# Kernel optimization log

Measured on AMD Instinct MI355X. Metric: run time of the kernel, lower is better.

Reference implementation:

```python
import jax, jax.numpy as jnp
import numpy as np

POOL = 7        # adaptive max pool output size
STRIDE = 16.0   # feature stride of VGG16 conv5


def _bin_masks(lo, hi, size, nbins=POOL):
    """Boolean masks [R, nbins, size]: pixel p belongs to adaptive-pool bin i
    of the region [lo, hi). PyTorch AdaptiveMaxPool2d bin boundaries:
    start = floor(i*L/n), end = ceil((i+1)*L/n), L = hi - lo."""
    L = hi - lo                                   # [R]
    i = jnp.arange(nbins, dtype=jnp.int32)
    starts = lo[:, None] + (i[None, :] * L[:, None]) // nbins          # [R, nbins]
    ends = lo[:, None] + ((i[None, :] + 1) * L[:, None] + nbins - 1) // nbins
    pos = jnp.arange(size, dtype=jnp.int32)
    return (pos[None, None, :] >= starts[..., None]) & (pos[None, None, :] < ends[..., None])


def roi_pool(x, rois):
    """x: [1,C,H,W]; rois: [R,4] = (y1,x1,y2,x2) in image pixels.
    Returns [R, C, POOL, POOL], matching the per-ROI slice + AdaptiveMaxPool2d loop."""
    xf = x[0]                                     # [C,H,W]
    C, H, W = xf.shape
    h0 = (rois[:, 0] / STRIDE).astype(jnp.int32)
    h1 = (rois[:, 2] / STRIDE).astype(jnp.int32) + 1
    w0 = (rois[:, 1] / STRIDE).astype(jnp.int32)
    w1 = (rois[:, 3] / STRIDE).astype(jnp.int32) + 1
    mH = _bin_masks(h0, h1, H)                    # [R,7,H]
    mW = _bin_masks(w0, w1, W)                    # [R,7,W]
    NEG = jnp.finfo(xf.dtype).min
    # reduce over W per w-bin (small fixed loop over 7 bins keeps memory bounded)
    colmax = jnp.stack(
        [jnp.where(mW[:, wb][:, None, None, :], xf[None], NEG).max(-1) for wb in range(POOL)],
        axis=-1)                                  # [R,C,H,7]
    # reduce over H per h-bin
    pooled = jnp.stack(
        [jnp.where(mH[:, hb][:, None, :, None], colmax, NEG).max(2) for hb in range(POOL)],
        axis=2)                                   # [R,C,7,7]
    return pooled


def setup_inputs() -> dict:
    key = jax.random.key(0)
    ks = jax.random.split(key, 10)
    H_img, W_img = 16 * 37, 16 * 50
    x = jax.random.normal(ks[0], (1, 512, 37, 50), dtype=jnp.float32)
    R = 128
    y1 = jax.random.uniform(ks[1], (R,), minval=0.0, maxval=H_img - 32.0)
    x1 = jax.random.uniform(ks[2], (R,), minval=0.0, maxval=W_img - 32.0)
    hh = jax.random.uniform(ks[3], (R,), minval=16.0, maxval=256.0)
    ww = jax.random.uniform(ks[4], (R,), minval=16.0, maxval=256.0)
    y2 = jnp.minimum(y1 + hh, H_img - 1.0)
    x2 = jnp.minimum(x1 + ww, W_img - 1.0)
    rois = jnp.stack([y1, x1, y2, x2], axis=1).astype(jnp.float32)
    D_in, D_h = 512 * POOL * POOL, 4096
    n_class = 21
    W1 = jax.random.normal(ks[5], (D_in, D_h), dtype=jnp.float32) * 0.01
    b1 = jnp.zeros((D_h,), jnp.float32)
    W2 = jax.random.normal(ks[6], (D_h, D_h), dtype=jnp.float32) * 0.01
    b2 = jnp.zeros((D_h,), jnp.float32)
    Wloc = jax.random.normal(ks[7], (D_h, n_class * 4), dtype=jnp.float32) * 0.001
    bloc = jnp.zeros((n_class * 4,), jnp.float32)
    Wscore = jax.random.normal(ks[8], (D_h, n_class), dtype=jnp.float32) * 0.01
    bscore = jnp.zeros((n_class,), jnp.float32)
    return {"x": x, "rois": rois, "W1": W1, "b1": b1, "W2": W2, "b2": b2,
            "Wloc": Wloc, "bloc": bloc, "Wscore": Wscore, "bscore": bscore}


def reference(x, rois, W1, b1, W2, b2, Wloc, bloc, Wscore, bscore):
    pooled = roi_pool(x, rois)                    # [R,512,7,7]
    flat = pooled.reshape(pooled.shape[0], -1)    # [R,25088]
    fc6 = jax.nn.relu(flat @ W1 + b1)
    fc7 = jax.nn.relu(fc6 @ W2 + b2)
    roi_locs = fc7 @ Wloc + bloc                  # [R, n_class*4]
    roi_scores = fc7 @ Wscore + bscore            # [R, n_class]
    return roi_locs, roi_scores
```

## Files before the change

### kernel.cpp

```cpp
#include <hip/hip_runtime.h>
#include <hip/hip_bf16.h>


typedef __attribute__((ext_vector_type(8))) short bf16x8;
typedef __attribute__((ext_vector_type(4))) float f32x4;
typedef __attribute__((ext_vector_type(4))) short s16x4;

typedef const __attribute__((address_space(1))) void gvoid;
typedef __attribute__((address_space(3))) void lvoid;
#define GLD_LDS16(gp, lp) __builtin_amdgcn_global_load_lds((gvoid*)(gp), (lvoid*)(lp), 16, 0, 0)

#define WAITV8() { asm volatile("s_waitcnt vmcnt(8)" ::: "memory"); __builtin_amdgcn_sched_barrier(0); }
#define WAITV0() { asm volatile("s_waitcnt vmcnt(0)" ::: "memory"); __builtin_amdgcn_sched_barrier(0); }
#define BAR() { __builtin_amdgcn_sched_barrier(0); __builtin_amdgcn_s_barrier(); __builtin_amdgcn_sched_barrier(0); }

static __device__ __forceinline__ short f2bf(float f) {
  unsigned u = __builtin_bit_cast(unsigned, f);
  u += 0x7fffu + ((u >> 16) & 1u);
  return (short)(u >> 16);
}

__global__ __launch_bounds__(256) void roipool_kernel(
    const float* __restrict__ x, const float* __restrict__ rois,
    __hip_bfloat16* __restrict__ A) {
  const int cg = blockIdx.x;
  const int r  = blockIdx.y;
  const float y1 = rois[r*4+0], x1 = rois[r*4+1], y2 = rois[r*4+2], x2 = rois[r*4+3];
  const int h0 = (int)(y1 * 0.0625f);
  const int h1 = (int)(y2 * 0.0625f) + 1;
  const int w0 = (int)(x1 * 0.0625f);
  const int w1 = (int)(x2 * 0.0625f) + 1;
  const int Hh = h1 - h0, Ww = w1 - w0;
  const int n = Hh * Ww;
  __shared__ float tile[16][292];
  const int cl = threadIdx.x >> 4, i = threadIdx.x & 15;
  const int c = cg*16 + cl;
  const float* xc = x + c*1850 + h0*50 + w0;
  for (int p = i; p < n; p += 16) {
    int rr = p / Ww, cc = p - rr*Ww;
    tile[cl][p] = xc[rr*50 + cc];
  }
  __syncthreads();
  __hip_bfloat16* Arow = A + (size_t)r*25088 + c*49;
  for (int b = i; b < 49; b += 16) {
    int hb = b / 7, wb = b - hb*7;
    int rs = (hb*Hh)/7,  re = ((hb+1)*Hh + 6)/7;
    int cs = (wb*Ww)/7,  ce = ((wb+1)*Ww + 6)/7;
    float m = -3.402823466e38f;
    for (int rr2 = rs; rr2 < re; ++rr2)
      for (int cc2 = cs; cc2 < ce; ++cc2)
        m = fmaxf(m, tile[cl][rr2*Ww + cc2]);
    Arow[b] = __float2bfloat16(m);
  }
}

__global__ __launch_bounds__(256) void gemm_kernel(
    const __hip_bfloat16* __restrict__ A,
    const float* __restrict__ B,
    float* __restrict__ part,
    int K, int KC) {
  __shared__ short lA[2][8192];
  __shared__ float lB[2][4096];
  const int t = threadIdx.x;
  const int w = t >> 6, l = t & 63;
  const int bid = blockIdx.x;
  const int s  = bid & 7;
  const int nb = bid >> 3;
  const int kc0 = s * KC;
  const int Arow_bytes = K * 2;

  int aoff[4], boff[4];
#pragma unroll
  for (int p = 0; p < 4; ++p) {
    int o = (p*256 + t) * 16;
    int oa = o ^ (((o >> 7) & 7) << 4);
    aoff[p] = (oa >> 7) * Arow_bytes + (oa & 127);
    int ob = o ^ (((o >> 11) & 1) << 6);
    boff[p] = (ob >> 8) * 16384 + (ob & 255);
  }
  const int r15 = l & 15, kh = l >> 4;
  const int xa = (r15 & 7) << 4;
  const int aoj0 = r15*128 + ((kh*16) ^ xa);
  const int aoj1 = r15*128 + (((64) + kh*16) ^ xa);
  const int bo0  = ((kh*8)*256 + (w*16 + r15)*4) ^ ((kh & 1) << 6);

  const char* Ak = (const char*)A + kc0*2;
  const char* Bk = (const char*)B + (size_t)kc0*16384 + nb*256;

  f32x4 acc[8] = {};
  const int steps = KC >> 6;
  int cur = 0;

#pragma unroll
  for (int p = 0; p < 4; ++p) {
    GLD_LDS16(Ak + aoff[p], (char*)lA[0] + (p*256 + w*64)*16);
    GLD_LDS16(Bk + boff[p], (char*)lB[0] + (p*256 + w*64)*16);
  }
  Ak += 128; Bk += 64 * 16384;

  for (int st = 0; st < steps; ++st) {
    if (st + 1 < steps) {
      char* dA = (char*)lA[cur ^ 1];
      char* dB = (char*)lB[cur ^ 1];
#pragma unroll
      for (int p = 0; p < 4; ++p) {
        GLD_LDS16(Ak + aoff[p], dA + (p*256 + w*64)*16);
        GLD_LDS16(Bk + boff[p], dB + (p*256 + w*64)*16);
      }
      Ak += 128; Bk += 64 * 16384;
      WAITV8();
    } else {
      WAITV0();
    }
    BAR();
    const char* lAb = (const char*)lA[cur];
    const char* lBb = (const char*)lB[cur];
#pragma unroll
    for (int j = 0; j < 2; ++j) {
      const int ao = j ? aoj1 : aoj0;
      const int bo = (j ? 8192 : 0) + bo0;
      float bf[8];
#pragma unroll
      for (int i2 = 0; i2 < 8; ++i2)
        bf[i2] = *(const float*)(lBb + bo + i2*256);
      bf16x8 bfrag;
#pragma unroll
      for (int i2 = 0; i2 < 8; ++i2) bfrag[i2] = f2bf(bf[i2]);
#pragma unroll
      for (int mf = 0; mf < 8; ++mf) {
        bf16x8 afrag = *(const bf16x8*)(lAb + mf*2048 + ao);
        acc[mf] = __builtin_amdgcn_mfma_f32_16x16x32_bf16(afrag, bfrag, acc[mf], 0, 0, 0);
      }
    }
    BAR();
    cur ^= 1;
  }
  const int n = nb*64 + w*16 + r15;
  float* prow = part + (size_t)s*524288 + n;
#pragma unroll
  for (int mf = 0; mf < 8; ++mf) {
    int m0 = mf*16 + kh*4;
#pragma unroll
    for (int q = 0; q < 4; ++q)
      prow[(m0 + q)*4096] = acc[mf][q];
  }
}

__global__ __launch_bounds__(256) void reduce_kernel(
    const float* __restrict__ part, const float* __restrict__ bias,
    short* __restrict__ outp) {
  const int idx = (blockIdx.x*256 + threadIdx.x) * 4;
  f32x4 sum = {};
#pragma unroll
  for (int s2 = 0; s2 < 8; ++s2)
    sum += *(const f32x4*)(part + (size_t)s2*524288 + idx);
  sum += *(const f32x4*)(bias + (idx & 4095));
  s16x4 o;
#pragma unroll
  for (int q = 0; q < 4; ++q) o[q] = f2bf(fmaxf(sum[q], 0.f));
  *(s16x4*)(outp + idx) = o;
}

__global__ __launch_bounds__(512) void final_kernel(
    const float* __restrict__ part, const float* __restrict__ b2,
    const float* __restrict__ Wloc, const float* __restrict__ bloc,
    const float* __restrict__ Wscore, const float* __restrict__ bscore,
    float* __restrict__ out) {
  __shared__ float row[4096];
  __shared__ float psum[4][128];
  const int r = blockIdx.x, t = threadIdx.x;
  for (int ci = t; ci < 1024; ci += 512) {
    f32x4 sum = {};
#pragma unroll
    for (int s2 = 0; s2 < 8; ++s2)
      sum += *(const f32x4*)(part + (size_t)s2*524288 + r*4096 + ci*4);
    sum += *(const f32x4*)(b2 + ci*4);
    f32x4 o;
#pragma unroll
    for (int q = 0; q < 4; ++q) o[q] = fmaxf(sum[q], 0.f);
    *(f32x4*)&row[ci*4] = o;
  }
  __syncthreads();
  const int c = t & 127, ks = t >> 7;
  float acc = 0.f;
  if (c < 105) {
    const float* W; int stride, cc;
    if (c < 84) { W = Wloc; stride = 84; cc = c; }
    else        { W = Wscore; stride = 21; cc = c - 84; }
    const int k0 = ks * 1024;
#pragma unroll 4
    for (int k = k0; k < k0 + 1024; ++k)
      acc = fmaf(row[k], W[(size_t)k*stride + cc], acc);
  }
  psum[ks][c] = acc;
  __syncthreads();
  if (ks == 0 && c < 105) {
    float v = psum[0][c] + psum[1][c] + psum[2][c] + psum[3][c];
    if (c < 84) out[(size_t)r*84 + c] = v + bloc[c];
    else        out[10752 + (size_t)r*21 + (c - 84)] = v + bscore[c - 84];
  }
}

extern "C" void kernel_launch(void* const* d_in, const int* in_sizes, int n_in,
                              void* d_out, int out_size, void* d_ws, size_t ws_size,
                              hipStream_t stream) {
  const float* x      = (const float*)d_in[0];
  const float* rois   = (const float*)d_in[1];
  const float* W1     = (const float*)d_in[2];
  const float* b1     = (const float*)d_in[3];
  const float* W2     = (const float*)d_in[4];
  const float* b2     = (const float*)d_in[5];
  const float* Wloc   = (const float*)d_in[6];
  const float* bloc   = (const float*)d_in[7];
  const float* Wscore = (const float*)d_in[8];
  const float* bscore = (const float*)d_in[9];
  float* out = (float*)d_out;

  char* ws = (char*)d_ws;
  __hip_bfloat16* Apool = (__hip_bfloat16*)(ws);
  short*          fc6   = (short*)(ws + 6422528);
  float*          part  = (float*)(ws + 9568256);

  roipool_kernel<<<dim3(32, 128), 256, 0, stream>>>(x, rois, Apool);
  gemm_kernel<<<512, 256, 0, stream>>>(Apool, W1, part, 25088, 3136);
  reduce_kernel<<<512, 256, 0, stream>>>(part, b1, fc6);
  gemm_kernel<<<512, 256, 0, stream>>>((const __hip_bfloat16*)fc6, W2, part, 4096, 512);
  final_kernel<<<128, 512, 0, stream>>>(part, b2, Wloc, bloc, Wscore, bscore, out);
}
```

Measured before the change: 253.5 us.

## Use wider-N, shorter-K tiles and 16-way split-K for the fc6 GEMM

Adds a dedicated fc6 GEMM kernel whose tiles are 128 columns wide with a 32-deep K step, and which splits K 16 ways instead of 8. Each A fragment now feeds two MFMAs, so A is read from LDS and global memory half as often per output. The A swizzle and B layout are adjusted to match. In exchange there are twice as many partial-sum planes to write and reduce, and the reduce kernel now sums 16 planes.

```diff
diff --git a/kernel.cpp b/kernel.cpp
--- a/kernel.cpp
+++ b/kernel.cpp
@@ -11,6 +11,7 @@
 #define GLD_LDS16(gp, lp) __builtin_amdgcn_global_load_lds((gvoid*)(gp), (lvoid*)(lp), 16, 0, 0)
 
 #define WAITV8() { asm volatile("s_waitcnt vmcnt(8)" ::: "memory"); __builtin_amdgcn_sched_barrier(0); }
+#define WAITV6() { asm volatile("s_waitcnt vmcnt(6)" ::: "memory"); __builtin_amdgcn_sched_barrier(0); }
 #define WAITV0() { asm volatile("s_waitcnt vmcnt(0)" ::: "memory"); __builtin_amdgcn_sched_barrier(0); }
 #define BAR() { __builtin_amdgcn_sched_barrier(0); __builtin_amdgcn_s_barrier(); __builtin_amdgcn_sched_barrier(0); }
 
@@ -54,6 +55,101 @@
   }
 }
 
+__global__ __launch_bounds__(256) void gemm1_kernel(
+    const __hip_bfloat16* __restrict__ A,
+    const float* __restrict__ B,
+    float* __restrict__ part) {
+  __shared__ short lA[2][4096];
+  __shared__ float lB[2][4096];
+  const int t = threadIdx.x;
+  const int w = t >> 6, l = t & 63;
+  const int bid = blockIdx.x;
+  const int s  = bid & 15;
+  const int nb = bid >> 4;
+  const int kc0 = s * 1568;
+  const int Arow_bytes = 25088 * 2;
+
+  int aoff[2], boff[4];
+#pragma unroll
+  for (int p = 0; p < 2; ++p) {
+    int o = (p*256 + t) * 16;
+    int oa = o ^ (((o >> 7) & 3) << 4);
+    aoff[p] = (oa >> 6) * Arow_bytes + (oa & 63);
+  }
+#pragma unroll
+  for (int p = 0; p < 4; ++p) {
+    int o = (p*256 + t) * 16;
+    int ob = o ^ (((o >> 12) & 1) << 6);
+    boff[p] = (ob >> 9) * 16384 + (ob & 511);
+  }
+  const int r15 = l & 15, kh = l >> 4;
+  const int axor = ((r15 >> 1) & 3) << 4;
+  const int ao0 = r15*64 + ((kh*16) ^ axor);
+  const int bo0 = ((kh*8)*512 + (w*32 + r15)*4)      ^ ((kh & 1) << 6);
+  const int bo1 = ((kh*8)*512 + (w*32 + 16 + r15)*4) ^ ((kh & 1) << 6);
+
+  const char* Ak = (const char*)A + kc0*2;
+  const char* Bk = (const char*)B + (size_t)kc0*16384 + nb*512;
+
+  f32x4 acc[8][2] = {};
+  int cur = 0;
+#pragma unroll
+  for (int p = 0; p < 2; ++p)
+    GLD_LDS16(Ak + aoff[p], (char*)lA[0] + (p*256 + w*64)*16);
+#pragma unroll
+  for (int p = 0; p < 4; ++p)
+    GLD_LDS16(Bk + boff[p], (char*)lB[0] + (p*256 + w*64)*16);
+  Ak += 64; Bk += (size_t)32*16384;
+
+  for (int st = 0; st < 49; ++st) {
+    if (st + 1 < 49) {
+      char* dA = (char*)lA[cur ^ 1];
+      char* dB = (char*)lB[cur ^ 1];
+#pragma unroll
+      for (int p = 0; p < 2; ++p)
+        GLD_LDS16(Ak + aoff[p], dA + (p*256 + w*64)*16);
+#pragma unroll
+      for (int p = 0; p < 4; ++p)
+        GLD_LDS16(Bk + boff[p], dB + (p*256 + w*64)*16);
+      Ak += 64; Bk += (size_t)32*16384;
+      WAITV6();
+    } else {
+      WAITV0();
+    }
+    BAR();
+    const char* lAb = (const char*)lA[cur];
+    const char* lBb = (const char*)lB[cur];
+    float bf0[8], bf1[8];
+#pragma unroll
+    for (int i2 = 0; i2 < 8; ++i2) {
+      bf0[i2] = *(const float*)(lBb + bo0 + i2*512);
+      bf1[i2] = *(const float*)(lBb + bo1 + i2*512);
+    }
+    bf16x8 bfr0, bfr1;
+#pragma unroll
+    for (int i2 = 0; i2 < 8; ++i2) { bfr0[i2] = f2bf(bf0[i2]); bfr1[i2] = f2bf(bf1[i2]); }
+#pragma unroll
+    for (int mf = 0; mf < 8; ++mf) {
+      bf16x8 afrag = *(const bf16x8*)(lAb + mf*1024 + ao0);
+      acc[mf][0] = __builtin_amdgcn_mfma_f32_16x16x32_bf16(afrag, bfr0, acc[mf][0], 0, 0, 0);
+      acc[mf][1] = __builtin_amdgcn_mfma_f32_16x16x32_bf16(afrag, bfr1, acc[mf][1], 0, 0, 0);
+    }
+    BAR();
+    cur ^= 1;
+  }
+  const int n0 = nb*128 + w*32 + r15;
+  float* prow = part + (size_t)s*524288 + n0;
+#pragma unroll
+  for (int mf = 0; mf < 8; ++mf) {
+    int m0 = mf*16 + kh*4;
+#pragma unroll
+    for (int q = 0; q < 4; ++q) {
+      prow[(m0 + q)*4096]      = acc[mf][0][q];
+      prow[(m0 + q)*4096 + 16] = acc[mf][1][q];
+    }
+  }
+}
+
 __global__ __launch_bounds__(256) void gemm_kernel(
     const __hip_bfloat16* __restrict__ A,
     const float* __restrict__ B,
@@ -152,7 +248,7 @@
   const int idx = (blockIdx.x*256 + threadIdx.x) * 4;
   f32x4 sum = {};
 #pragma unroll
-  for (int s2 = 0; s2 < 8; ++s2)
+  for (int s2 = 0; s2 < 16; ++s2)
     sum += *(const f32x4*)(part + (size_t)s2*524288 + idx);
   sum += *(const f32x4*)(bias + (idx & 4095));
   s16x4 o;
@@ -222,7 +318,7 @@
   float*          part  = (float*)(ws + 9568256);
 
   roipool_kernel<<<dim3(32, 128), 256, 0, stream>>>(x, rois, Apool);
-  gemm_kernel<<<512, 256, 0, stream>>>(Apool, W1, part, 25088, 3136);
+  gemm1_kernel<<<512, 256, 0, stream>>>(Apool, W1, part);
   reduce_kernel<<<512, 256, 0, stream>>>(part, b1, fc6);
   gemm_kernel<<<512, 256, 0, stream>>>((const __hip_bfloat16*)fc6, W2, part, 4096, 512);
   final_kernel<<<128, 512, 0, stream>>>(part, b2, Wloc, bloc, Wscore, bscore, out);
```

Result: faster. 243.9 us (median of 2 runs) (-3.8%).

## Widen GEMM N-tile to 128 and double split-K to 16 slices

Applied to the files above, without the earlier changes.

The GEMM tile changes from 128x64 with a 64-deep K step to 128x128 with a 32-deep K step. Each wave now computes two 16-column MFMA fragments, so every A fragment read from LDS is reused twice. Split-K goes from 8 to 16 slices, which keeps 512 blocks, and the reduce and final kernels now sum 16 partials. The goal is better A reuse and less A traffic per output. The cost is twice the partial-sum writes and reads, and the workspace for partials grows to 16 slices, which may overrun the allocation.

```diff
diff --git a/kernel.cpp b/kernel.cpp
--- a/kernel.cpp
+++ b/kernel.cpp
@@ -10,7 +10,7 @@
 typedef __attribute__((address_space(3))) void lvoid;
 #define GLD_LDS16(gp, lp) __builtin_amdgcn_global_load_lds((gvoid*)(gp), (lvoid*)(lp), 16, 0, 0)
 
-#define WAITV8() { asm volatile("s_waitcnt vmcnt(8)" ::: "memory"); __builtin_amdgcn_sched_barrier(0); }
+#define WAITV6() { asm volatile("s_waitcnt vmcnt(6)" ::: "memory"); __builtin_amdgcn_sched_barrier(0); }
 #define WAITV0() { asm volatile("s_waitcnt vmcnt(0)" ::: "memory"); __builtin_amdgcn_sched_barrier(0); }
 #define BAR() { __builtin_amdgcn_sched_barrier(0); __builtin_amdgcn_s_barrier(); __builtin_amdgcn_sched_barrier(0); }
 
@@ -54,95 +54,99 @@
   }
 }
 
-__global__ __launch_bounds__(256) void gemm_kernel(
+__global__ __launch_bounds__(256) void gemm_ktile(
     const __hip_bfloat16* __restrict__ A,
     const float* __restrict__ B,
     float* __restrict__ part,
-    int K, int KC) {
-  __shared__ short lA[2][8192];
+    int K, int KC, int steps) {
+  __shared__ short lA[2][4096];
   __shared__ float lB[2][4096];
   const int t = threadIdx.x;
   const int w = t >> 6, l = t & 63;
   const int bid = blockIdx.x;
-  const int s  = bid & 7;
-  const int nb = bid >> 3;
+  const int s  = bid & 15;
+  const int nb = bid >> 4;
   const int kc0 = s * KC;
   const int Arow_bytes = K * 2;
 
-  int aoff[4], boff[4];
+  int aoff[2], boff[4];
+#pragma unroll
+  for (int p = 0; p < 2; ++p) {
+    int o = (p*256 + t) * 16;
+    int oa = o ^ (((o >> 7) & 3) << 4);
+    aoff[p] = (oa >> 6) * Arow_bytes + (oa & 63);
+  }
 #pragma unroll
   for (int p = 0; p < 4; ++p) {
     int o = (p*256 + t) * 16;
-    int oa = o ^ (((o >> 7) & 7) << 4);
-    aoff[p] = (oa >> 7) * Arow_bytes + (oa & 127);
-    int ob = o ^ (((o >> 11) & 1) << 6);
-    boff[p] = (ob >> 8) * 16384 + (ob & 255);
+    int ob = o ^ (((o >> 12) & 1) << 6);
+    boff[p] = (ob >> 9) * 16384 + (ob & 511);
   }
   const int r15 = l & 15, kh = l >> 4;
-  const int xa = (r15 & 7) << 4;
-  const int aoj0 = r15*128 + ((kh*16) ^ xa);
-  const int aoj1 = r15*128 + (((64) + kh*16) ^ xa);
-  const int bo0  = ((kh*8)*256 + (w*16 + r15)*4) ^ ((kh & 1) << 6);
+  const int axor = ((r15 >> 1) & 3) << 4;
+  const int ao0 = r15*64 + ((kh*16) ^ axor);
+  const int bo0 = ((kh*8)*512 + (w*32 + r15)*4)      ^ ((kh & 1) << 6);
+  const int bo1 = ((kh*8)*512 + (w*32 + 16 + r15)*4) ^ ((kh & 1) << 6);
 
   const char* Ak = (const char*)A + kc0*2;
-  const char* Bk = (const char*)B + (size_t)kc0*16384 + nb*256;
-
-  f32x4 acc[8] = {};
-  const int steps = KC >> 6;
+  const char* Bk = (const char*)B + (size_t)kc0*16384 + nb*512;
+
+  f32x4 acc[8][2] = {};
   int cur = 0;
-
-#pragma unroll
-  for (int p = 0; p < 4; ++p) {
+#pragma unroll
+  for (int p = 0; p < 2; ++p)
     GLD_LDS16(Ak + aoff[p], (char*)lA[0] + (p*256 + w*64)*16);
+#pragma unroll
+  for (int p = 0; p < 4; ++p)
     GLD_LDS16(Bk + boff[p], (char*)lB[0] + (p*256 + w*64)*16);
-  }
-  Ak += 128; Bk += 64 * 16384;
+  Ak += 64; Bk += (size_t)32*16384;
 
   for (int st = 0; st < steps; ++st) {
     if (st + 1 < steps) {
       char* dA = (char*)lA[cur ^ 1];
       char* dB = (char*)lB[cur ^ 1];
 #pragma unroll
-      for (int p = 0; p < 4; ++p) {
+      for (int p = 0; p < 2; ++p)
         GLD_LDS16(Ak + aoff[p], dA + (p*256 + w*64)*16);
+#pragma unroll
+      for (int p = 0; p < 4; ++p)
         GLD_LDS16(Bk + boff[p], dB + (p*256 + w*64)*16);
-      }
-      Ak += 128; Bk += 64 * 16384;
-      WAITV8();
+      Ak += 64; Bk += (size_t)32*16384;
+      WAITV6();
     } else {
       WAITV0();
     }
     BAR();
     const char* lAb = (const char*)lA[cur];
     const char* lBb = (const char*)lB[cur];
-#pragma unroll
-    for (int j = 0; j < 2; ++j) {
-      const int ao = j ? aoj1 : aoj0;
-      const int bo = (j ? 8192 : 0) + bo0;
-      float bf[8];
-#pragma unroll
-      for (int i2 = 0; i2 < 8; ++i2)
-        bf[i2] = *(const float*)(lBb + bo + i2*256);
-      bf16x8 bfrag;
-#pragma unroll
-      for (int i2 = 0; i2 < 8; ++i2) bfrag[i2] = f2bf(bf[i2]);
-#pragma unroll
-      for (int mf = 0; mf < 8; ++mf) {
-        bf16x8 afrag = *(const bf16x8*)(lAb + mf*2048 + ao);
-        acc[mf] = __builtin_amdgcn_mfma_f32_16x16x32_bf16(afrag, bfrag, acc[mf], 0, 0, 0);
-      }
+    float bf0[8], bf1[8];
+#pragma unroll
+    for (int i2 = 0; i2 < 8; ++i2) {
+      bf0[i2] = *(const float*)(lBb + bo0 + i2*512);
+      bf1[i2] = *(const float*)(lBb + bo1 + i2*512);
+    }
+    bf16x8 bfr0, bfr1;
+#pragma unroll
+    for (int i2 = 0; i2 < 8; ++i2) { bfr0[i2] = f2bf(bf0[i2]); bfr1[i2] = f2bf(bf1[i2]); }
+#pragma unroll
+    for (int mf = 0; mf < 8; ++mf) {
+      bf16x8 afrag = *(const bf16x8*)(lAb + mf*1024 + ao0);
+      acc[mf][0] = __builtin_amdgcn_mfma_f32_16x16x32_bf16(afrag, bfr0, acc[mf][0], 0, 0, 0);
+      acc[mf][1] = __builtin_amdgcn_mfma_f32_16x16x32_bf16(afrag, bfr1, acc[mf][1], 0, 0, 0);
     }
     BAR();
     cur ^= 1;
   }
-  const int n = nb*64 + w*16 + r15;
-  float* prow = part + (size_t)s*524288 + n;
+  const int n0 = nb*128 + w*32 + r15;
+  float* prow = part + (size_t)s*524288 + n0;
 #pragma unroll
   for (int mf = 0; mf < 8; ++mf) {
     int m0 = mf*16 + kh*4;
 #pragma unroll
-    for (int q = 0; q < 4; ++q)
-      prow[(m0 + q)*4096] = acc[mf][q];
+    for (int q = 0; q < 4; ++q) {
+      prow[(m0 + q)*4096]      = acc[mf][0][q];
+      prow[(m0 + q)*4096 + 16] = acc[mf][1][q];
+    }
   }
 }
 
@@ -152,7 +156,7 @@
   const int idx = (blockIdx.x*256 + threadIdx.x) * 4;
   f32x4 sum = {};
 #pragma unroll
-  for (int s2 = 0; s2 < 8; ++s2)
+  for (int s2 = 0; s2 < 16; ++s2)
     sum += *(const f32x4*)(part + (size_t)s2*524288 + idx);
   sum += *(const f32x4*)(bias + (idx & 4095));
   s16x4 o;
@@ -172,7 +176,7 @@
   for (int ci = t; ci < 1024; ci += 512) {
     f32x4 sum = {};
 #pragma unroll
-    for (int s2 = 0; s2 < 8; ++s2)
+    for (int s2 = 0; s2 < 16; ++s2)
       sum += *(const f32x4*)(part + (size_t)s2*524288 + r*4096 + ci*4);
     sum += *(const f32x4*)(b2 + ci*4);
     f32x4 o;
@@ -222,8 +226,8 @@
   float*          part  = (float*)(ws + 9568256);
 
   roipool_kernel<<<dim3(32, 128), 256, 0, stream>>>(x, rois, Apool);
-  gemm_kernel<<<512, 256, 0, stream>>>(Apool, W1, part, 25088, 3136);
+  gemm_ktile<<<512, 256, 0, stream>>>(Apool, W1, part, 25088, 1568, 49);
   reduce_kernel<<<512, 256, 0, stream>>>(part, b1, fc6);
-  gemm_kernel<<<512, 256, 0, stream>>>((const __hip_bfloat16*)fc6, W2, part, 4096, 512);
+  gemm_ktile<<<512, 256, 0, stream>>>((const __hip_bfloat16*)fc6, W2, part, 4096, 256, 8);
   final_kernel<<<128, 512, 0, stream>>>(part, b2, Wloc, bloc, Wscore, bscore, out);
 }
```

New measurement: 247.5 us. 2.4% less time.
